# Kernel optimization log

Measured on AMD Instinct MI355X. Metric: run time of the kernel, lower is better.

Reference implementation:

```python
import math
import jax, jax.numpy as jnp
import numpy as np

DIM = 4096
N_HEADS = 32
N_KV_HEADS = 8
HEAD_DIM = DIM // N_HEADS        # 128
N_REP = N_HEADS // N_KV_HEADS    # 4
BSZ = 1
SEQ = 2048
ROPE_THETA = 500000.0


def setup_inputs() -> dict:
    key = jax.random.key(0)
    ks = jax.random.split(key, 5)
    scale = 1.0 / math.sqrt(DIM)
    x = jax.random.normal(ks[0], (BSZ, SEQ, DIM), dtype=jnp.float32)
    wq = jax.random.normal(ks[1], (N_HEADS * HEAD_DIM, DIM), dtype=jnp.float32) * scale
    wk = jax.random.normal(ks[2], (N_KV_HEADS * HEAD_DIM, DIM), dtype=jnp.float32) * scale
    wv = jax.random.normal(ks[3], (N_KV_HEADS * HEAD_DIM, DIM), dtype=jnp.float32) * scale
    wo = jax.random.normal(ks[4], (N_HEADS * HEAD_DIM, DIM), dtype=jnp.float32).T * scale
    wo = jnp.asarray(wo)  # [DIM, N_HEADS*HEAD_DIM] like nn.Linear(in=heads*hd, out=dim).weight
    # RoPE tables: freqs_cis[t, j] = exp(i * t * theta^{-2j/head_dim}), j in [0, head_dim/2)
    inv_freq = 1.0 / (ROPE_THETA ** (np.arange(0, HEAD_DIM, 2, dtype=np.float32) / HEAD_DIM))
    t = np.arange(SEQ, dtype=np.float32)
    ang = np.outer(t, inv_freq)  # [SEQ, HEAD_DIM//2]
    freqs_cos = jnp.asarray(np.cos(ang), dtype=jnp.float32)
    freqs_sin = jnp.asarray(np.sin(ang), dtype=jnp.float32)
    # additive causal mask [SEQ, SEQ]
    mask = jnp.where(jnp.tril(jnp.ones((SEQ, SEQ), dtype=bool)), 0.0, -1e9).astype(jnp.float32)
    return {"x": x, "wq": wq, "wk": wk, "wv": wv, "wo": wo,
            "freqs_cos": freqs_cos, "freqs_sin": freqs_sin, "mask": mask}


def _apply_rope(xh, cos, sin):
    # xh: [b, s, h, head_dim]; cos/sin: [s, head_dim//2]
    b, s, h, d = xh.shape
    xr = xh.reshape(b, s, h, d // 2, 2)
    x0, x1 = xr[..., 0], xr[..., 1]
    c = cos[None, :, None, :]
    sn = sin[None, :, None, :]
    o0 = x0 * c - x1 * sn
    o1 = x0 * sn + x1 * c
    return jnp.stack([o0, o1], axis=-1).reshape(b, s, h, d)


def reference(x, wq, wk, wv, wo, freqs_cos, freqs_sin, mask):
    bsz, seqlen, _ = x.shape
    xq = (x @ wq.T).reshape(bsz, seqlen, N_HEADS, HEAD_DIM)
    xk = (x @ wk.T).reshape(bsz, seqlen, N_KV_HEADS, HEAD_DIM)
    xv = (x @ wv.T).reshape(bsz, seqlen, N_KV_HEADS, HEAD_DIM)
    xq = _apply_rope(xq, freqs_cos, freqs_sin)
    xk = _apply_rope(xk, freqs_cos, freqs_sin)
    # repeat_kv (GQA expansion)
    keys = jnp.repeat(xk, N_REP, axis=2)    # [b, s, N_HEADS, hd]
    values = jnp.repeat(xv, N_REP, axis=2)
    scores = jnp.einsum('bqhd,bkhd->bhqk', xq, keys) / math.sqrt(HEAD_DIM)
    scores = scores + mask[None, None, :, :]
    scores = jax.nn.softmax(scores.astype(jnp.float32), axis=-1).astype(xq.dtype)
    out = jnp.einsum('bhqk,bkhd->bqhd', scores, values)
    out = out.reshape(bsz, seqlen, N_HEADS * HEAD_DIM)
    return out @ wo.T
```

## Files before the change

kernel.cpp:

```cpp
#include <hip/hip_runtime.h>
#include <math.h>
#include <stdint.h>
#include <stddef.h>


typedef __attribute__((ext_vector_type(8))) short bf16x8;
typedef __attribute__((ext_vector_type(4))) short bf16x4;
typedef __attribute__((ext_vector_type(4))) float f32x4;
typedef unsigned short u16;

#define NEG_BIG (-1.0e9f)
#define MFMA32(a, b, c) __builtin_amdgcn_mfma_f32_16x16x32_bf16(a, b, c, 0, 0, 0)

__device__ __forceinline__ float bf2f(u16 b) {
    return __uint_as_float(((unsigned int)b) << 16);
}
__device__ __forceinline__ u16 f2bf(float f) {
    unsigned int u = __float_as_uint(f);
    u += 0x7fff + ((u >> 16) & 1);
    return (u16)(u >> 16);
}
__device__ __forceinline__ void gld_lds16(short* lds, const u16* g) {
    __builtin_amdgcn_global_load_lds(
        (const __attribute__((address_space(1))) void*)g,
        (__attribute__((address_space(3))) void*)lds, 16, 0, 0);
}

__global__ __launch_bounds__(256) void cvt_bf16(const float* __restrict__ src,
                                                u16* __restrict__ dst, int n) {
    int i = (blockIdx.x * blockDim.x + threadIdx.x) * 8;
    if (i >= n) return;
    float4 a, b;
    __builtin_memcpy(&a, src + i, 16);
    __builtin_memcpy(&b, src + i + 4, 16);
    bf16x8 o;
    o[0] = (short)f2bf(a.x); o[1] = (short)f2bf(a.y);
    o[2] = (short)f2bf(a.z); o[3] = (short)f2bf(a.w);
    o[4] = (short)f2bf(b.x); o[5] = (short)f2bf(b.y);
    o[6] = (short)f2bf(b.z); o[7] = (short)f2bf(b.w);
    __builtin_memcpy(dst + i, &o, 16);
}


#define G8_STGA(bf_, ks_, kt_)                                               \
    {                                                                        \
        _Pragma("unroll") for (int r_ = 0; r_ < RA; ++r_)                    \
            gld_lds16(Ad + (bf_) * AT + (ks_) * AH + r_ * 4096,              \
                      Ag + gK * r_ + (size_t)(kt_) * 64 + (ks_) * 32);       \
    }
#define G8_STGB(bf_, ks_, kt_)                                               \
    {                                                                        \
        _Pragma("unroll") for (int r_ = 0; r_ < RB; ++r_)                    \
            gld_lds16(Bd + (bf_) * BT + (ks_) * BH + r_ * 4096,              \
                      Bg + gK * r_ + (size_t)(kt_) * 64 + (ks_) * 32);       \
    }
#define G8_PHASE(bf_, ks_, mh_, RDB_, STAGE_, WAIT_)                         \
    {                                                                        \
        if (RDB_) {                                                          \
            _Pragma("unroll") for (int n_ = 0; n_ < 4; ++n_)                 \
                __builtin_memcpy(&bfr[n_], Bs + (bf_) * BT + (ks_) * BH +    \
                                               bbase + n_ * 512, 16);        \
        }                                                                    \
        _Pragma("unroll") for (int i_ = 0; i_ < 4; ++i_)                     \
            __builtin_memcpy(&af[i_], S + (bf_) * AT + (ks_) * AH + abase +  \
                                          ((mh_) * 64 + i_ * 16) * 32, 16);  \
        STAGE_;                                                              \
        __builtin_amdgcn_s_barrier();                                        \
        asm volatile("s_waitcnt lgkmcnt(0)" ::: "memory");                   \
        __builtin_amdgcn_s_setprio(1);                                       \
        _Pragma("unroll") for (int i_ = 0; i_ < 4; ++i_)                     \
            _Pragma("unroll") for (int n_ = 0; n_ < 4; ++n_)                 \
                acc[(mh_) * 4 + i_][n_] =                                    \
                    MFMA32(af[i_], bfr[n_], acc[(mh_) * 4 + i_][n_]);        \
        __builtin_amdgcn_s_setprio(0);                                       \
        WAIT_;                                                               \
        __builtin_amdgcn_s_barrier();                                        \
    }

template <int BM, int BN, int MH, int OUT>
__device__ __forceinline__ void gemm8p(const u16* __restrict__ A,
                                       const u16* __restrict__ B,
                                       void* __restrict__ C,
                                       int mb, int nb, int N, int K,
                                       short* __restrict__ S) {
    constexpr int AT = BM * 64, BT = BN * 64;
    constexpr int AH = BM * 32, BH = BN * 32;
    constexpr int RA = BM / 128, RB = BN / 128;
    short* const Bs = S + 2 * AT;

    const int t = threadIdx.x;
    const int lane = t & 63, l15 = lane & 15, quad = lane >> 4;
    const int wid = t >> 6, wr = wid >> 2, wc = wid & 3;

    const int srow = t >> 2;
    const int cs = (t & 3) ^ ((t >> 3) & 3);
    const u16* const Ag = A + (size_t)(mb * BM + srow) * K + cs * 8;
    const u16* const Bg = B + (size_t)(nb * BN + srow) * K + cs * 8;
    short* const Ad = S + t * 8;
    short* const Bd = Bs + t * 8;
    const size_t gK = (size_t)128 * K;

    const int swz = (quad ^ ((l15 >> 1) & 3)) * 8;
    const int abase = (wr * (BM / 2) + l15) * 32 + swz;
    const int bbase = (wc * 64 + l15) * 32 + swz;

    f32x4 acc[MH * 4][4] = {};
    bf16x8 af[4], bfr[4];

    G8_STGA(0, 0, 0); G8_STGB(0, 0, 0);
    G8_STGA(0, 1, 0); G8_STGB(0, 1, 0);
    G8_STGA(1, 0, 1); G8_STGB(1, 0, 1);
    if constexpr (MH == 2) {
        asm volatile("s_waitcnt vmcnt(4)" ::: "memory");
    } else {
        asm volatile("s_waitcnt vmcnt(6)" ::: "memory");
    }
    __builtin_amdgcn_s_barrier();

    const int nIt = K >> 7;
    if constexpr (MH == 2) {
        for (int it = 0; it < nIt; ++it) {
            const int k0 = 2 * it, k1 = k0 + 1;
            const bool nl = (it < nIt - 1);
            G8_PHASE(0, 0, 0, true,  G8_STGA(1, 1, k1), );
            G8_PHASE(0, 0, 1, false, G8_STGB(1, 1, k1), );
            G8_PHASE(0, 1, 0, true,  if (nl) G8_STGA(0, 0, k0 + 2), );
            G8_PHASE(0, 1, 1, false, if (nl) G8_STGB(0, 0, k0 + 2),
                     if (nl) { asm volatile("s_waitcnt vmcnt(4)" ::: "memory"); }
                     else    { asm volatile("s_waitcnt vmcnt(0)" ::: "memory"); });
            G8_PHASE(1, 0, 0, true,  if (nl) G8_STGA(0, 1, k0 + 2), );
            G8_PHASE(1, 0, 1, false, if (nl) G8_STGB(0, 1, k0 + 2), );
            G8_PHASE(1, 1, 0, true,  if (nl) G8_STGA(1, 0, k1 + 2), );
            G8_PHASE(1, 1, 1, false, if (nl) G8_STGB(1, 0, k1 + 2),
                     if (nl) { asm volatile("s_waitcnt vmcnt(4)" ::: "memory"); });
        }
    } else {
        for (int it = 0; it < nIt - 1; ++it) {
            const int k0 = 2 * it, k1 = k0 + 1;
            G8_PHASE(0, 0, 0, true, { G8_STGA(1, 1, k1); G8_STGB(1, 1, k1); },
                     asm volatile("s_waitcnt vmcnt(6)" ::: "memory"));
            G8_PHASE(0, 1, 0, true, { G8_STGA(0, 0, k0 + 2); G8_STGB(0, 0, k0 + 2); },
                     asm volatile("s_waitcnt vmcnt(6)" ::: "memory"));
            G8_PHASE(1, 0, 0, true, { G8_STGA(0, 1, k0 + 2); G8_STGB(0, 1, k0 + 2); },
                     asm volatile("s_waitcnt vmcnt(6)" ::: "memory"));
            G8_PHASE(1, 1, 0, true, { G8_STGA(1, 0, k1 + 2); G8_STGB(1, 0, k1 + 2); },
                     asm volatile("s_waitcnt vmcnt(6)" ::: "memory"));
        }
        {
            const int k1 = (K >> 6) - 1;
            G8_PHASE(0, 0, 0, true, { G8_STGA(1, 1, k1); G8_STGB(1, 1, k1); },
                     asm volatile("s_waitcnt vmcnt(6)" ::: "memory"));
            G8_PHASE(0, 1, 0, true, ,
                     asm volatile("s_waitcnt vmcnt(3)" ::: "memory"));
            G8_PHASE(1, 0, 0, true, ,
                     asm volatile("s_waitcnt vmcnt(0)" ::: "memory"));
            G8_PHASE(1, 1, 0, true, , );
        }
    }

#pragma unroll
    for (int i8 = 0; i8 < MH * 4; ++i8) {
        const int rowb = mb * BM + wr * (BM / 2) + (i8 >> 2) * 64 +
                         (i8 & 3) * 16 + quad * 4;
#pragma unroll
        for (int j = 0; j < 4; ++j) {
            const int col = nb * BN + wc * 64 + j * 16 + l15;
            if (OUT == 2) {
                bf16x4 v;
#pragma unroll
                for (int r = 0; r < 4; ++r) v[r] = (short)f2bf(acc[i8][j][r]);
                __builtin_memcpy((u16*)C + (size_t)col * 2048 + rowb, &v, 8);
            } else if (OUT == 1) {
#pragma unroll
                for (int r = 0; r < 4; ++r)
                    ((float*)C)[(size_t)(rowb + r) * N + col] = acc[i8][j][r];
            } else {
#pragma unroll
                for (int r = 0; r < 4; ++r)
                    ((u16*)C)[(size_t)(rowb + r) * N + col] =
                        f2bf(acc[i8][j][r]);
            }
        }
    }
}

__global__ __launch_bounds__(512, 2) void qkv_proj8(
    const u16* __restrict__ x,
    const u16* __restrict__ wq, const u16* __restrict__ wk,
    const u16* __restrict__ wv,
    u16* __restrict__ Q, u16* __restrict__ Kc, u16* __restrict__ Vt) {
    __shared__ __align__(16) short S[65536];
    const int mb = blockIdx.x, y = blockIdx.y;
    if (y < 16)
        gemm8p<256, 256, 2, 0>(x, wq, Q, mb, y, 4096, 4096, S);
    else if (y < 20)
        gemm8p<256, 256, 2, 0>(x, wk, Kc, mb, y - 16, 1024, 4096, S);
    else
        gemm8p<256, 256, 2, 2>(x, wv, Vt, mb, y - 20, 1024, 4096, S);
}

__global__ __launch_bounds__(512, 2) void oproj8(
    const u16* __restrict__ A, const u16* __restrict__ wo,
    float* __restrict__ out) {
    __shared__ __align__(16) short S[49152];
    gemm8p<128, 256, 1, 1>(A, wo, out, blockIdx.x, blockIdx.y, 4096, 4096, S);
}

__global__ void rope_kernel(u16* __restrict__ X,
                            const float* __restrict__ cosb,
                            const float* __restrict__ sinb, int nheads) {
    int idx = blockIdx.x * blockDim.x + threadIdx.x;
    int total = 2048 * nheads * 64;
    if (idx >= total) return;
    int i = idx % 64;
    int h = (idx / 64) % nheads;
    int s = idx / (64 * nheads);
    u16* p = X + (size_t)s * nheads * 128 + h * 128 + 2 * i;
    float x0 = bf2f(p[0]), x1 = bf2f(p[1]);
    float c = cosb[s * 64 + i], sn = sinb[s * 64 + i];
    p[0] = f2bf(x0 * c - x1 * sn);
    p[1] = f2bf(x0 * sn + x1 * c);
}

__device__ __forceinline__ int kswz(int row, int cs) {
    int f = (row & 3) | ((row & 8) >> 1);
    return row * 128 + ((cs ^ f) << 3);
}

template <bool MASKED>
__device__ __forceinline__ void fa_step_lds(
    const short* __restrict__ Kl, const short* __restrict__ Vl,
    int kb, int q0, int l15, int quad,
    const int (&koff)[8], const int (&voff)[8],
    const bf16x8 (&qf)[4], f32x4 (&o)[8], float& m, float& l) {
    const float scale = 0.08838834764831845f;

    bf16x8 kf[8];
#pragma unroll
    for (int i = 0; i < 8; ++i) __builtin_memcpy(&kf[i], Kl + koff[i], 16);
    f32x4 s0 = {0, 0, 0, 0}, s1 = {0, 0, 0, 0};
#pragma unroll
    for (int c = 0; c < 4; ++c) {
        s0 = MFMA32(kf[c], qf[c], s0);
        s1 = MFMA32(kf[4 + c], qf[c], s1);
    }

    bf16x8 vf[8];
#pragma unroll
    for (int n = 0; n < 8; ++n) __builtin_memcpy(&vf[n], Vl + voff[n], 16);

    float sv0[4], sv1[4];
    const int q = q0 + l15;
#pragma unroll
    for (int r = 0; r < 4; ++r) {
        sv0[r] = s0[r] * scale;
        sv1[r] = s1[r] * scale;
        if (MASKED) {
            if (kb + 8 * quad + r > q) sv0[r] = NEG_BIG;
            if (kb + 8 * quad + 4 + r > q) sv1[r] = NEG_BIG;
        }
    }

    float mx = fmaxf(fmaxf(fmaxf(sv0[0], sv0[1]), fmaxf(sv0[2], sv0[3])),
                     fmaxf(fmaxf(sv1[0], sv1[1]), fmaxf(sv1[2], sv1[3])));
    mx = fmaxf(mx, __shfl_xor(mx, 16));
    mx = fmaxf(mx, __shfl_xor(mx, 32));

    float alpha = 1.0f;
    if (!__all(mx <= m + 8.0f)) {
        float mnew = fmaxf(m, mx);
        alpha = __expf(m - mnew);
        float aO[4];
#pragma unroll
        for (int r = 0; r < 4; ++r) aO[r] = __shfl(alpha, quad * 20 + r);
#pragma unroll
        for (int n = 0; n < 8; ++n)
#pragma unroll
            for (int r = 0; r < 4; ++r) o[n][r] *= aO[r];
        m = mnew;
    }

    float p0[4], p1[4], sum = 0.f;
#pragma unroll
    for (int r = 0; r < 4; ++r) {
        p0[r] = __expf(sv0[r] - m);
        p1[r] = __expf(sv1[r] - m);
        sum += p0[r] + p1[r];
    }
    sum += __shfl_xor(sum, 16);
    sum += __shfl_xor(sum, 32);
    l = l * alpha + sum;

    bf16x8 pa;
#pragma unroll
    for (int r = 0; r < 4; ++r) {
        pa[r] = (short)f2bf(p0[r]);
        pa[4 + r] = (short)f2bf(p1[r]);
    }

#pragma unroll
    for (int n = 0; n < 8; ++n) o[n] = MFMA32(pa, vf[n], o[n]);
}

__device__ __forceinline__ void fa_task(
    const u16* __restrict__ Q, const u16* __restrict__ Kc,
    const u16* __restrict__ Vt, u16* __restrict__ O,
    short* __restrict__ Kl0, short* __restrict__ Vl0,
    int q0, int nbt, int h, int kvh, int t) {
    const int lane = t & 63;
    const int l15 = lane & 15, quad = lane >> 4;

    bf16x8 qf[4];
    const u16* qp = Q + (size_t)(q0 + l15) * 4096 + h * 128 + quad * 8;
#pragma unroll
    for (int c = 0; c < 4; ++c) __builtin_memcpy(&qf[c], qp + c * 32, 16);

    const u16* ksrc[2]; short* kdst[2];
    const u16* vsrc[2]; short* vdst[2];
#pragma unroll
    for (int r = 0; r < 2; ++r) {
        int row = (t >> 4) + 16 * r;
        int slot = t & 15;
        int f = (row & 3) | ((row & 8) >> 1);
        int cks = slot ^ f;
        ksrc[r] = Kc + (size_t)row * 1024 + kvh * 128 + cks * 8;
        kdst[r] = Kl0 + (t + 256 * r) * 8;
        int rowv = (t >> 2) + 64 * r;
        int csv = (t & 3) ^ ((t >> 3) & 3);
        vsrc[r] = Vt + (size_t)(kvh * 128 + rowv) * 2048 + csv * 8;
        vdst[r] = Vl0 + (t + 256 * r) * 8;
    }

    const int rk0 = 8 * (l15 >> 2) + (l15 & 3);
    int koff[8], voff[8];
#pragma unroll
    for (int c = 0; c < 4; ++c) {
        koff[c] = kswz(rk0, quad + c * 4);
        koff[4 + c] = kswz(rk0 + 4, quad + c * 4);
    }
    const int vswz = (quad ^ ((l15 >> 1) & 3)) * 8;
#pragma unroll
    for (int n = 0; n < 8; ++n) voff[n] = (n * 16 + l15) * 32 + vswz;

    f32x4 o[8] = {};
    float m = NEG_BIG, l = 0.f;
    const int my_nb = (q0 + 47) / 32;

    {
        gld_lds16(kdst[0], ksrc[0]);
        gld_lds16(kdst[1], ksrc[1]);
        gld_lds16(vdst[0], vsrc[0]);
        gld_lds16(vdst[1], vsrc[1]);
    }
    __syncthreads();

    for (int ib = 0; ib < nbt; ++ib) {
        if (ib + 1 < nbt) {
            int kb = (ib + 1) * 32;
            int bo = ((ib + 1) & 1) * 4096;
            gld_lds16(kdst[0] + bo, ksrc[0] + (size_t)kb * 1024);
            gld_lds16(kdst[1] + bo, ksrc[1] + (size_t)kb * 1024);
            gld_lds16(vdst[0] + bo, vsrc[0] + kb);
            gld_lds16(vdst[1] + bo, vsrc[1] + kb);
        }
        if (ib < my_nb) {
            const short* Kl = Kl0 + (ib & 1) * 4096;
            const short* Vl = Vl0 + (ib & 1) * 4096;
            if (ib == my_nb - 1)
                fa_step_lds<true>(Kl, Vl, ib * 32, q0, l15, quad, koff, voff,
                                  qf, o, m, l);
            else
                fa_step_lds<false>(Kl, Vl, ib * 32, q0, l15, quad, koff, voff,
                                   qf, o, m, l);
        }
        __syncthreads();
    }

    float inv[4];
#pragma unroll
    for (int r = 0; r < 4; ++r) inv[r] = 1.f / __shfl(l, quad * 20 + r);
#pragma unroll
    for (int n = 0; n < 8; ++n)
#pragma unroll
        for (int r = 0; r < 4; ++r) {
            int row = q0 + quad * 4 + r;
            O[(size_t)row * 4096 + h * 128 + n * 16 + l15] =
                f2bf(o[n][r] * inv[r]);
        }
}

__global__ __launch_bounds__(256) void flash_attn(
    const u16* __restrict__ Q, const u16* __restrict__ Kc,
    const u16* __restrict__ Vt, u16* __restrict__ O) {
    __shared__ __align__(16) short Kl[2 * 32 * 128];
    __shared__ __align__(16) short Vl[2 * 128 * 32];
    const int pp = blockIdx.x;
    const int h = blockIdx.y;
    const int kvh = h >> 2;
    const int t = threadIdx.x, wave = t >> 6;
    fa_task(Q, Kc, Vt, O, Kl, Vl, pp * 64 + wave * 16, 2 * pp + 2, h, kvh, t);
    const int tb = 31 - pp;
    fa_task(Q, Kc, Vt, O, Kl, Vl, tb * 64 + (3 - wave) * 16, 2 * tb + 2, h,
            kvh, t);
}

extern "C" void kernel_launch(void* const* d_in, const int* in_sizes, int n_in,
                              void* d_out, int out_size, void* d_ws,
                              size_t ws_size, hipStream_t stream) {
    const float* x  = (const float*)d_in[0];
    const float* wq = (const float*)d_in[1];
    const float* wk = (const float*)d_in[2];
    const float* wv = (const float*)d_in[3];
    const float* wo = (const float*)d_in[4];
    const float* fc = (const float*)d_in[5];
    const float* fs = (const float*)d_in[6];
    float* out = (float*)d_out;

    const int NX = 2048 * 4096;
    const int NQW = 4096 * 4096;
    const int NKW = 1024 * 4096;
    const int NKV = 2048 * 1024;

    u16* Q   = (u16*)d_ws;
    u16* Kc  = Q   + NX;
    u16* Vt  = Kc  + NKV;
    u16* Ao  = Vt  + NKV;
    u16* xb  = Ao  + NX;
    u16* wqb = xb  + NX;
    u16* wkb = wqb + NQW;
    u16* wvb = wkb + NKW;
    u16* wob = wvb + NKW;

    cvt_bf16<<<NX / (256 * 8), 256, 0, stream>>>(x, xb, NX);
    cvt_bf16<<<NQW / (256 * 8), 256, 0, stream>>>(wq, wqb, NQW);
    cvt_bf16<<<NKW / (256 * 8), 256, 0, stream>>>(wk, wkb, NKW);
    cvt_bf16<<<NKW / (256 * 8), 256, 0, stream>>>(wv, wvb, NKW);
    cvt_bf16<<<NQW / (256 * 8), 256, 0, stream>>>(wo, wob, NQW);

    qkv_proj8<<<dim3(8, 24), 512, 0, stream>>>(xb, wqb, wkb, wvb, Q, Kc, Vt);
    rope_kernel<<<(2048 * 32 * 64 + 255) / 256, 256, 0, stream>>>(Q, fc, fs, 32);
    rope_kernel<<<(2048 * 8 * 64 + 255) / 256, 256, 0, stream>>>(Kc, fc, fs, 8);
    flash_attn<<<dim3(16, 32), 256, 0, stream>>>(Q, Kc, Vt, Ao);
    oproj8<<<dim3(16, 16), 512, 0, stream>>>(Ao, wob, out);
}
```

Measured before the change: 500.2 us.

## Merge conversion and RoPE launches, swizzle GEMM block order, add sched barriers

```diff
diff --git a/kernel.cpp b/kernel.cpp
--- a/kernel.cpp
+++ b/kernel.cpp
@@ -11,6 +11,7 @@
 
 #define NEG_BIG (-1.0e9f)
 #define MFMA32(a, b, c) __builtin_amdgcn_mfma_f32_16x16x32_bf16(a, b, c, 0, 0, 0)
+#define SFENCE() __builtin_amdgcn_sched_barrier(0)
 
 __device__ __forceinline__ float bf2f(u16 b) {
     return __uint_as_float(((unsigned int)b) << 16);
@@ -26,19 +27,29 @@
         (__attribute__((address_space(3))) void*)lds, 16, 0, 0);
 }
 
-__global__ __launch_bounds__(256) void cvt_bf16(const float* __restrict__ src,
-                                                u16* __restrict__ dst, int n) {
-    int i = (blockIdx.x * blockDim.x + threadIdx.x) * 8;
-    if (i >= n) return;
-    float4 a, b;
-    __builtin_memcpy(&a, src + i, 16);
-    __builtin_memcpy(&b, src + i + 4, 16);
+__global__ __launch_bounds__(256) void cvt_all(
+    const float* __restrict__ x, const float* __restrict__ wq,
+    const float* __restrict__ wk, const float* __restrict__ wv,
+    const float* __restrict__ wo,
+    u16* __restrict__ xb, u16* __restrict__ wqb, u16* __restrict__ wkb,
+    u16* __restrict__ wvb, u16* __restrict__ wob) {
+    const int b = blockIdx.x;
+    const float* s; u16* d; int off;
+    if (b < 4096)       { s = x;  d = xb;  off = b; }
+    else if (b < 12288) { s = wq; d = wqb; off = b - 4096; }
+    else if (b < 14336) { s = wk; d = wkb; off = b - 12288; }
+    else if (b < 16384) { s = wv; d = wvb; off = b - 14336; }
+    else                { s = wo; d = wob; off = b - 16384; }
+    const int i = off * 2048 + threadIdx.x * 8;
+    float4 a, c;
+    __builtin_memcpy(&a, s + i, 16);
+    __builtin_memcpy(&c, s + i + 4, 16);
     bf16x8 o;
     o[0] = (short)f2bf(a.x); o[1] = (short)f2bf(a.y);
     o[2] = (short)f2bf(a.z); o[3] = (short)f2bf(a.w);
-    o[4] = (short)f2bf(b.x); o[5] = (short)f2bf(b.y);
-    o[6] = (short)f2bf(b.z); o[7] = (short)f2bf(b.w);
-    __builtin_memcpy(dst + i, &o, 16);
+    o[4] = (short)f2bf(c.x); o[5] = (short)f2bf(c.y);
+    o[6] = (short)f2bf(c.z); o[7] = (short)f2bf(c.w);
+    __builtin_memcpy(d + i, &o, 16);
 }
 
 
@@ -65,14 +76,17 @@
             __builtin_memcpy(&af[i_], S + (bf_) * AT + (ks_) * AH + abase +  \
                                           ((mh_) * 64 + i_ * 16) * 32, 16);  \
         STAGE_;                                                              \
+        SFENCE();                                                            \
         __builtin_amdgcn_s_barrier();                                        \
         asm volatile("s_waitcnt lgkmcnt(0)" ::: "memory");                   \
+        SFENCE();                                                            \
         __builtin_amdgcn_s_setprio(1);                                       \
         _Pragma("unroll") for (int i_ = 0; i_ < 4; ++i_)                     \
             _Pragma("unroll") for (int n_ = 0; n_ < 4; ++n_)                 \
                 acc[(mh_) * 4 + i_][n_] =                                    \
                     MFMA32(af[i_], bfr[n_], acc[(mh_) * 4 + i_][n_]);        \
         __builtin_amdgcn_s_setprio(0);                                       \
+        SFENCE();                                                            \
         WAIT_;                                                               \
         __builtin_amdgcn_s_barrier();                                        \
     }
@@ -190,7 +204,9 @@
     const u16* __restrict__ wv,
     u16* __restrict__ Q, u16* __restrict__ Kc, u16* __restrict__ Vt) {
     __shared__ __align__(16) short S[65536];
-    const int mb = blockIdx.x, y = blockIdx.y;
+    const int lid = blockIdx.x;
+    const int swzb = (lid & 7) * 24 + (lid >> 3);
+    const int mb = swzb & 7, y = swzb >> 3;
     if (y < 16)
         gemm8p<256, 256, 2, 0>(x, wq, Q, mb, y, 4096, 4096, S);
     else if (y < 20)
@@ -203,21 +219,26 @@
     const u16* __restrict__ A, const u16* __restrict__ wo,
     float* __restrict__ out) {
     __shared__ __align__(16) short S[49152];
-    gemm8p<128, 256, 1, 1>(A, wo, out, blockIdx.x, blockIdx.y, 4096, 4096, S);
-}
-
-__global__ void rope_kernel(u16* __restrict__ X,
-                            const float* __restrict__ cosb,
-                            const float* __restrict__ sinb, int nheads) {
-    int idx = blockIdx.x * blockDim.x + threadIdx.x;
-    int total = 2048 * nheads * 64;
-    if (idx >= total) return;
-    int i = idx % 64;
-    int h = (idx / 64) % nheads;
-    int s = idx / (64 * nheads);
-    u16* p = X + (size_t)s * nheads * 128 + h * 128 + 2 * i;
-    float x0 = bf2f(p[0]), x1 = bf2f(p[1]);
-    float c = cosb[s * 64 + i], sn = sinb[s * 64 + i];
+    const int lid = blockIdx.x;
+    const int logical = (lid & 7) * 32 + (lid >> 3);
+    const int mb = logical & 15, nb = logical >> 4;
+    gemm8p<128, 256, 1, 1>(A, wo, out, mb, nb, 4096, 4096, S);
+}
+
+__global__ __launch_bounds__(256) void rope_all(
+    u16* __restrict__ Q, u16* __restrict__ Kc,
+    const float* __restrict__ cosb, const float* __restrict__ sinb) {
+    const int idx = blockIdx.x * blockDim.x + threadIdx.x;
+    const int i = idx & 63;
+    const int hh = (idx >> 6) % 40;
+    const int s = (idx >> 6) / 40;
+    u16* p;
+    if (hh < 32)
+        p = Q + (size_t)s * 4096 + hh * 128 + 2 * i;
+    else
+        p = Kc + (size_t)s * 1024 + (hh - 32) * 128 + 2 * i;
+    const float x0 = bf2f(p[0]), x1 = bf2f(p[1]);
+    const float c = cosb[s * 64 + i], sn = sinb[s * 64 + i];
     p[0] = f2bf(x0 * c - x1 * sn);
     p[1] = f2bf(x0 * sn + x1 * c);
 }
@@ -431,15 +452,10 @@
     u16* wvb = wkb + NKW;
     u16* wob = wvb + NKW;
 
-    cvt_bf16<<<NX / (256 * 8), 256, 0, stream>>>(x, xb, NX);
-    cvt_bf16<<<NQW / (256 * 8), 256, 0, stream>>>(wq, wqb, NQW);
-    cvt_bf16<<<NKW / (256 * 8), 256, 0, stream>>>(wk, wkb, NKW);
-    cvt_bf16<<<NKW / (256 * 8), 256, 0, stream>>>(wv, wvb, NKW);
-    cvt_bf16<<<NQW / (256 * 8), 256, 0, stream>>>(wo, wob, NQW);
-
-    qkv_proj8<<<dim3(8, 24), 512, 0, stream>>>(xb, wqb, wkb, wvb, Q, Kc, Vt);
-    rope_kernel<<<(2048 * 32 * 64 + 255) / 256, 256, 0, stream>>>(Q, fc, fs, 32);
-    rope_kernel<<<(2048 * 8 * 64 + 255) / 256, 256, 0, stream>>>(Kc, fc, fs, 8);
+    cvt_all<<<24576, 256, 0, stream>>>(x, wq, wk, wv, wo,
+                                       xb, wqb, wkb, wvb, wob);
+    qkv_proj8<<<192, 512, 0, stream>>>(xb, wqb, wkb, wvb, Q, Kc, Vt);
+    rope_all<<<20480, 256, 0, stream>>>(Q, Kc, fc, fs);
     flash_attn<<<dim3(16, 32), 256, 0, stream>>>(Q, Kc, Vt, Ao);
-    oproj8<<<dim3(16, 16), 512, 0, stream>>>(Ao, wob, out);
-}
+    oproj8<<<256, 512, 0, stream>>>(Ao, wob, out);
+}
```

New measurement: 487.2 us. 2.6% less time.
